# Optimization experiments

Measured on AMD Instinct MI355X. Metric: run time of the kernel, lower is better.

The kernel has to match this reference:

```python
import jax, jax.numpy as jnp
import numpy as np

B, T, C = 32, 128, 64
E, H = 8, 4            # feat_dim, num_heads
D = E // H             # head_dim = 2
HID = 32               # hidden_dim


def setup_inputs() -> dict:
    key = jax.random.key(0)
    ks = jax.random.split(key, 20)
    s = 0.1
    return {
        "x": jax.random.normal(ks[0], (B, T, C), jnp.float32),
        # input_proj: Linear(C, C)
        "W_in": jax.random.normal(ks[1], (C, C), jnp.float32) * s,
        "b_in": jax.random.normal(ks[2], (C,), jnp.float32) * s,
        # time_step_score: Linear(C, C//4) -> GELU -> Linear(C//4, 1) -> Sigmoid
        "W_ts1": jax.random.normal(ks[3], (C // 4, C), jnp.float32) * s,
        "b_ts1": jax.random.normal(ks[4], (C // 4,), jnp.float32) * s,
        "W_ts2": jax.random.normal(ks[5], (1, C // 4), jnp.float32) * s,
        "b_ts2": jax.random.normal(ks[6], (1,), jnp.float32) * s,
        # per-channel GRU(1 -> E): torch gate order (r, z, n)
        "W_ih": jax.random.normal(ks[7], (C, 3 * E), jnp.float32) * s,      # input size 1
        "W_hh": jax.random.normal(ks[8], (C, 3 * E, E), jnp.float32) * s,
        "b_ih": jax.random.normal(ks[9], (C, 3 * E), jnp.float32) * s,
        "b_hh": jax.random.normal(ks[10], (C, 3 * E), jnp.float32) * s,
        # shared MultiheadAttention(E, 4): packed in_proj + out_proj
        "W_qkv": jax.random.normal(ks[11], (3 * E, E), jnp.float32) * s,
        "b_qkv": jax.random.normal(ks[12], (3 * E,), jnp.float32) * s,
        "W_o": jax.random.normal(ks[13], (E, E), jnp.float32) * s,
        "b_o": jax.random.normal(ks[14], (E,), jnp.float32) * s,
        # out_proj: Linear(C*E, HID)
        "W_out": jax.random.normal(ks[15], (HID, C * E), jnp.float32) * s,
        "b_out": jax.random.normal(ks[16], (HID,), jnp.float32) * s,
    }


def _forward(x, W_in, b_in, W_ts1, b_ts1, W_ts2, b_ts2,
             W_ih, W_hh, b_ih, b_hh, W_qkv, b_qkv, W_o, b_o, W_out, b_out):
    bs, ts, c = x.shape
    # time step importance: per-timestep MLP over the raw features
    h1 = jax.nn.gelu(jnp.einsum('btc,fc->btf', x, W_ts1) + b_ts1, approximate=False)
    ts_imp = jax.nn.sigmoid(jnp.einsum('btf,of->bto', h1, W_ts2) + b_ts2)[..., 0]  # [B,T]

    xp = jnp.einsum('btc,dc->btd', x, W_in) + b_in  # [B,T,C]

    # Batched per-channel GRU scan over time. state h: [B,C,E]
    def step(h, x_t):
        gi = x_t[:, :, None] * W_ih[None] + b_ih          # [B,C,3E]
        gh = jnp.einsum('bce,cge->bcg', h, W_hh) + b_hh   # [B,C,3E]
        ir, iz, inn = gi[..., :E], gi[..., E:2 * E], gi[..., 2 * E:]
        hr, hz, hn = gh[..., :E], gh[..., E:2 * E], gh[..., 2 * E:]
        r = jax.nn.sigmoid(ir + hr)
        z = jax.nn.sigmoid(iz + hz)
        n = jnp.tanh(inn + r * hn)
        h_new = (1.0 - z) * n + z * h
        return h_new, h_new

    h0 = jnp.zeros((bs, c, E), xp.dtype)
    _, hs = jax.lax.scan(step, h0, jnp.transpose(xp, (1, 0, 2)))  # [T,B,C,E]
    hs_bcte = jnp.transpose(hs, (1, 2, 0, 3))                     # [B,C,T,E]

    # Shared MHA applied independently per channel (batched over B*C)
    qkv = jnp.einsum('bcte,fe->bctf', hs_bcte, W_qkv) + b_qkv     # [B,C,T,3E]
    q, k, v = qkv[..., :E], qkv[..., E:2 * E], qkv[..., 2 * E:]
    def heads(t):
        return t.reshape(bs, c, ts, H, D)
    q, k, v = heads(q), heads(k), heads(v)
    scores = jnp.einsum('bcthd,bcshd->bchts', q, k) / np.sqrt(D)
    attn = jax.nn.softmax(scores, axis=-1)
    o = jnp.einsum('bchts,bcshd->bcthd', attn, v).reshape(bs, c, ts, E)
    attn_out = jnp.einsum('bcte,fe->bctf', o, W_o) + b_o          # [B,C,T,E]
    attention = jnp.transpose(attn_out, (0, 2, 1, 3))             # [B,T,C,E]

    out_flat = jnp.transpose(hs, (1, 0, 2, 3)).reshape(bs, ts, c * E)  # [B,T,C*E]
    out = jnp.einsum('btf,hf->bth', out_flat, W_out) + b_out           # [B,T,HID]

    feat_imp = jax.nn.sigmoid(attention.sum(axis=(1, 3)))   # [B,C]
    tsf_imp = jax.nn.sigmoid(attention.sum(axis=-1))        # [B,T,C]
    return out[:, -1, :], feat_imp, ts_imp, tsf_imp


def reference(x, W_in, b_in, W_ts1, b_ts1, W_ts2, b_ts2,
              W_ih, W_hh, b_ih, b_hh, W_qkv, b_qkv, W_o, b_o, W_out, b_out):
    return _forward(x, W_in, b_in, W_ts1, b_ts1, W_ts2, b_ts2,
                    W_ih, W_hh, b_ih, b_hh, W_qkv, b_qkv, W_o, b_o, W_out, b_out)
```

## Files before the change

### kernel.cpp

```cpp
#include <hip/hip_runtime.h>
#include <hip/hip_bf16.h>
#include <math.h>

#define B_ 32
#define T_ 128
#define C_ 64
#define E_ 8
#define HID_ 32

#define LOG2E 1.44269504088896341f

__device__ __forceinline__ float fast_rcp(float x) { return __builtin_amdgcn_rcpf(x); }
__device__ __forceinline__ float fast_exp2(float x) { return exp2f(x); }
__device__ __forceinline__ float fast_sigmoid(float x) {
    return fast_rcp(1.0f + fast_exp2(-LOG2E * x));
}
__device__ __forceinline__ float fast_tanh(float x) {
    float xc = __builtin_amdgcn_fmed3f(x, -15.0f, 15.0f);
    float t = fast_exp2(2.0f * LOG2E * xc);
    return (t - 1.0f) * fast_rcp(t + 1.0f);
}

template <int CTRL>
__device__ __forceinline__ float dppf(float v) {
    return __int_as_float(__builtin_amdgcn_update_dpp(
        __float_as_int(v), __float_as_int(v), CTRL, 0xF, 0xF, false));
}
#define QP_XOR1 0xB1
#define QP_XOR2 0x4E
#define QP_XOR3 0x1B
#define HALF_MIRROR 0x141

__global__ __launch_bounds__(64) void k_pre_ts(
    const float* __restrict__ x, const float* __restrict__ W_in, const float* __restrict__ b_in,
    const float* __restrict__ W_ts1, const float* __restrict__ b_ts1,
    const float* __restrict__ W_ts2, const float* __restrict__ b_ts2,
    float* __restrict__ xp, float* __restrict__ ts_imp)
{
    const int bt = blockIdx.x;
    const int tid = threadIdx.x;
    __shared__ __align__(16) float xs[C_];
    __shared__ float h1[16];
    if (tid < 16) ((float4*)xs)[tid] = ((const float4*)(x + bt * C_))[tid];
    __syncthreads();

    float a = b_in[tid];
    const float4* w4 = (const float4*)(W_in + tid * C_);
#pragma unroll
    for (int k4 = 0; k4 < 16; ++k4) {
        float4 xv = ((const float4*)xs)[k4];
        float4 wv = w4[k4];
        a = fmaf(xv.x, wv.x, a); a = fmaf(xv.y, wv.y, a);
        a = fmaf(xv.z, wv.z, a); a = fmaf(xv.w, wv.w, a);
    }
    xp[bt * C_ + tid] = a;

    if (tid < 16) {
        float s = b_ts1[tid];
#pragma unroll
        for (int k = 0; k < C_; ++k) s = fmaf(xs[k], W_ts1[tid * C_ + k], s);
        h1[tid] = 0.5f * s * (1.0f + erff(s * 0.70710678118654752f));
    }
    __syncthreads();
    if (tid == 0) {
        float s = b_ts2[0];
#pragma unroll
        for (int k = 0; k < 16; ++k) s = fmaf(h1[k], W_ts2[k], s);
        ts_imp[bt] = fast_sigmoid(s);
    }
}

__global__ __launch_bounds__(64) void k_gru(
    const float* __restrict__ xp, const float* __restrict__ W_ih, const float* __restrict__ W_hh,
    const float* __restrict__ b_ih, const float* __restrict__ b_hh,
    float* __restrict__ hs, float* __restrict__ fh)
{
    const int tid = threadIdx.x;
    const int ci = tid >> 3;
    const int e = tid & 7;
    const int chain = blockIdx.x * 8 + ci;
    const int c = chain & 63;

    __shared__ float xc[8][T_ + 1];

    const int c_base = (blockIdx.x & 7) * 8;
    const int bb = blockIdx.x >> 3;
    for (int idx = tid; idx < 8 * T_; idx += 64) {
        int cci = idx & 7, t = idx >> 3;
        xc[cci][t] = xp[(bb * T_ + t) * C_ + c_base + cci];
    }
    __syncthreads();

    float wr[8], wz[8], wn[8];
#pragma unroll
    for (int m = 0; m < 8; ++m) {
        const int j = e ^ m;
        wr[m] = W_hh[(c * 24 + 0  + e) * 8 + j];
        wz[m] = W_hh[(c * 24 + 8  + e) * 8 + j];
        wn[m] = W_hh[(c * 24 + 16 + e) * 8 + j];
    }
    const float wir = W_ih[c * 24 + e], wiz = W_ih[c * 24 + 8 + e], win = W_ih[c * 24 + 16 + e];
    const float cr = b_ih[c * 24 + e] + b_hh[c * 24 + e];
    const float cz = b_ih[c * 24 + 8 + e] + b_hh[c * 24 + 8 + e];
    const float bin_ = b_ih[c * 24 + 16 + e];
    const float bhn  = b_hh[c * 24 + 16 + e];

    float h = 0.0f;
    float* ho = hs + (size_t)chain * T_ * E_ + e;
    float xv = xc[ci][0];
    for (int t = 0; t < T_; ++t) {
        float xvn = xc[ci][t + 1];
        float p1 = dppf<QP_XOR1>(h);
        float p2 = dppf<QP_XOR2>(h);
        float p3 = dppf<QP_XOR3>(h);
        float p7 = dppf<HALF_MIRROR>(h);
        float p6 = dppf<HALF_MIRROR>(p1);
        float p5 = dppf<HALF_MIRROR>(p2);
        float p4 = dppf<HALF_MIRROR>(p3);
        const float pa[8] = {h, p1, p2, p3, p4, p5, p6, p7};

        float g0 = fmaf(pa[1], wr[1], pa[0] * wr[0]);
        float g1 = fmaf(pa[3], wr[3], pa[2] * wr[2]);
        float g2 = fmaf(pa[5], wr[5], pa[4] * wr[4]);
        float g3 = fmaf(pa[7], wr[7], pa[6] * wr[6]);
        float gr = fmaf(xv, wir, cr) + ((g0 + g1) + (g2 + g3));
        float z0 = fmaf(pa[1], wz[1], pa[0] * wz[0]);
        float z1 = fmaf(pa[3], wz[3], pa[2] * wz[2]);
        float z2 = fmaf(pa[5], wz[5], pa[4] * wz[4]);
        float z3 = fmaf(pa[7], wz[7], pa[6] * wz[6]);
        float gz = fmaf(xv, wiz, cz) + ((z0 + z1) + (z2 + z3));
        float n0 = fmaf(pa[1], wn[1], pa[0] * wn[0]);
        float n1 = fmaf(pa[3], wn[3], pa[2] * wn[2]);
        float n2 = fmaf(pa[5], wn[5], pa[4] * wn[4]);
        float n3 = fmaf(pa[7], wn[7], pa[6] * wn[6]);
        float hn = bhn + ((n0 + n1) + (n2 + n3));
        float gn = fmaf(xv, win, bin_);
        float r = fast_sigmoid(gr);
        float z = fast_sigmoid(gz);
        float nn = fast_tanh(fmaf(r, hn, gn));
        h = fmaf(z, h - nn, nn);
        ho[t * E_] = h;
        xv = xvn;
    }
    fh[chain * E_ + e] = h;
}

__global__ __launch_bounds__(256) void k_attn(
    const float* __restrict__ hs, const float* __restrict__ W_qkv, const float* __restrict__ b_qkv,
    const float* __restrict__ W_o, const float* __restrict__ b_o,
    float* __restrict__ feat_imp, float* __restrict__ tsf_imp)
{
    const int bc = blockIdx.x;
    const int b = bc >> 6, c = bc & 63;
    const int tid = threadIdx.x;
    const int t2 = tid & 63;
    const int sq = tid >> 6;

    __shared__ __align__(16) float ks[T_][E_];
    __shared__ __align__(16) float us[T_][4];
    __shared__ float qsT[E_][T_];
    __shared__ float pacc[3][T_][8];
    __shared__ float red[T_];

    const float qscale = 0.70710678118654752f * LOG2E;

    {
        const int row = (tid < 128) ? tid : (tid - 128);
        const float4* hp = (const float4*)(hs + (size_t)bc * T_ * E_ + row * E_);
        float4 h0 = hp[0], h1 = hp[1];
        float hr[E_] = {h0.x, h0.y, h0.z, h0.w, h1.x, h1.y, h1.z, h1.w};
        if (tid < 128) {
            float kv[E_];
#pragma unroll
            for (int f = 0; f < E_; ++f) {
                float a = b_qkv[E_ + f];
#pragma unroll
                for (int j = 0; j < E_; ++j) a = fmaf(hr[j], W_qkv[(E_ + f) * E_ + j], a);
                kv[f] = a;
            }
            ((float4*)&ks[row][0])[0] = make_float4(kv[0], kv[1], kv[2], kv[3]);
            ((float4*)&ks[row][0])[1] = make_float4(kv[4], kv[5], kv[6], kv[7]);
#pragma unroll
            for (int f = 0; f < E_; ++f) {
                float a = b_qkv[f];
#pragma unroll
                for (int j = 0; j < E_; ++j) a = fmaf(hr[j], W_qkv[f * E_ + j], a);
                qsT[f][row] = a * qscale;
            }
        } else {
            float ws[E_];
#pragma unroll
            for (int d = 0; d < E_; ++d) {
                float wv = 0.0f;
#pragma unroll
                for (int fp = 0; fp < E_; ++fp) wv += W_o[fp * E_ + d];
                ws[d] = wv;
            }
            float vv[E_];
#pragma unroll
            for (int f = 0; f < E_; ++f) {
                float a = b_qkv[2 * E_ + f];
#pragma unroll
                for (int j = 0; j < E_; ++j) a = fmaf(hr[j], W_qkv[(2 * E_ + f) * E_ + j], a);
                vv[f] = a;
            }
            float4 uu;
            uu.x = fmaf(vv[1], ws[1], vv[0] * ws[0]);
            uu.y = fmaf(vv[3], ws[3], vv[2] * ws[2]);
            uu.z = fmaf(vv[5], ws[5], vv[4] * ws[4]);
            uu.w = fmaf(vv[7], ws[7], vv[6] * ws[6]);
            *((float4*)&us[row][0]) = uu;
        }
    }
    __syncthreads();

    float q0[E_], q1[E_];
#pragma unroll
    for (int f = 0; f < E_; ++f) { q0[f] = qsT[f][t2]; q1[f] = qsT[f][t2 + 64]; }

    float l0[4] = {0.f,0.f,0.f,0.f}, S0[4] = {0.f,0.f,0.f,0.f};
    float l1[4] = {0.f,0.f,0.f,0.f}, S1[4] = {0.f,0.f,0.f,0.f};
    const float* kb = &ks[sq * 32][0];
    const float* ub = &us[sq * 32][0];
#pragma unroll 8
    for (int i = 0; i < 32; ++i) {
        float4 k0 = *(const float4*)(kb + i * 8);
        float4 k1 = *(const float4*)(kb + i * 8 + 4);
        float4 uu = *(const float4*)(ub + i * 4);
        float p00 = fast_exp2(fmaf(q0[1], k0.y, q0[0] * k0.x));
        float p01 = fast_exp2(fmaf(q0[3], k0.w, q0[2] * k0.z));
        float p02 = fast_exp2(fmaf(q0[5], k1.y, q0[4] * k1.x));
        float p03 = fast_exp2(fmaf(q0[7], k1.w, q0[6] * k1.z));
        float p10 = fast_exp2(fmaf(q1[1], k0.y, q1[0] * k0.x));
        float p11 = fast_exp2(fmaf(q1[3], k0.w, q1[2] * k0.z));
        float p12 = fast_exp2(fmaf(q1[5], k1.y, q1[4] * k1.x));
        float p13 = fast_exp2(fmaf(q1[7], k1.w, q1[6] * k1.z));
        l0[0] += p00; l0[1] += p01; l0[2] += p02; l0[3] += p03;
        l1[0] += p10; l1[1] += p11; l1[2] += p12; l1[3] += p13;
        S0[0] = fmaf(p00, uu.x, S0[0]); S0[1] = fmaf(p01, uu.y, S0[1]);
        S0[2] = fmaf(p02, uu.z, S0[2]); S0[3] = fmaf(p03, uu.w, S0[3]);
        S1[0] = fmaf(p10, uu.x, S1[0]); S1[1] = fmaf(p11, uu.y, S1[1]);
        S1[2] = fmaf(p12, uu.z, S1[2]); S1[3] = fmaf(p13, uu.w, S1[3]);
    }

    if (sq > 0) {
        float* pr = &pacc[sq - 1][t2][0];
#pragma unroll
        for (int i = 0; i < 4; ++i) { pr[i] = l0[i]; pr[4 + i] = S0[i]; }
        pr = &pacc[sq - 1][t2 + 64][0];
#pragma unroll
        for (int i = 0; i < 4; ++i) { pr[i] = l1[i]; pr[4 + i] = S1[i]; }
    }
    __syncthreads();

    if (sq == 0) {
        float bsum = 0.0f;
#pragma unroll
        for (int fp = 0; fp < E_; ++fp) bsum += b_o[fp];
#pragma unroll
        for (int qq = 0; qq < 3; ++qq) {
#pragma unroll
            for (int i = 0; i < 4; ++i) {
                l0[i] += pacc[qq][t2][i];       S0[i] += pacc[qq][t2][4 + i];
                l1[i] += pacc[qq][t2 + 64][i];  S1[i] += pacc[qq][t2 + 64][4 + i];
            }
        }
        float Sa = bsum, Sb = bsum;
#pragma unroll
        for (int hh = 0; hh < 4; ++hh) {
            Sa = fmaf(S0[hh], fast_rcp(l0[hh]), Sa);
            Sb = fmaf(S1[hh], fast_rcp(l1[hh]), Sb);
        }
        tsf_imp[(size_t)b * T_ * C_ + (size_t)t2 * C_ + c] = fast_sigmoid(Sa);
        tsf_imp[(size_t)b * T_ * C_ + (size_t)(t2 + 64) * C_ + c] = fast_sigmoid(Sb);
        red[t2] = Sa;
        red[t2 + 64] = Sb;
    }
    __syncthreads();
    for (int off = 64; off > 0; off >>= 1) {
        if (tid < off) red[tid] += red[tid + off];
        __syncthreads();
    }
    if (tid == 0) feat_imp[bc] = fast_sigmoid(red[0]);
}

__global__ __launch_bounds__(64) void k_out(
    const float* __restrict__ fh, const float* __restrict__ W_out, const float* __restrict__ b_out,
    float* __restrict__ out0)
{
    const int b = blockIdx.x;
    const int tid = threadIdx.x;
    __shared__ float hf[C_ * E_];
    const float4* src = (const float4*)(fh + (b * C_ + tid) * E_);
    float4* dst = (float4*)(hf + tid * E_);
    dst[0] = src[0];
    dst[1] = src[1];
    __syncthreads();
    if (tid < HID_) {
        float a = b_out[tid];
        const float* wo = W_out + tid * (C_ * E_);
        for (int k = 0; k < C_ * E_; ++k) a = fmaf(hf[k], wo[k], a);
        out0[b * HID_ + tid] = a;
    }
}

extern "C" void kernel_launch(void* const* d_in, const int* in_sizes, int n_in,
                              void* d_out, int out_size, void* d_ws, size_t ws_size,
                              hipStream_t stream) {
    (void)in_sizes; (void)n_in; (void)out_size; (void)ws_size;

    float* out0 = (float*)d_out;
    float* feat = out0 + B_ * HID_;
    float* tsim = feat + B_ * C_;
    float* tsf  = tsim + B_ * T_;

    const float* x     = (const float*)d_in[0];
    const float* W_in  = (const float*)d_in[1];
    const float* b_in  = (const float*)d_in[2];
    const float* W_ts1 = (const float*)d_in[3];
    const float* b_ts1 = (const float*)d_in[4];
    const float* W_ts2 = (const float*)d_in[5];
    const float* b_ts2 = (const float*)d_in[6];
    const float* W_ih  = (const float*)d_in[7];
    const float* W_hh  = (const float*)d_in[8];
    const float* b_ih  = (const float*)d_in[9];
    const float* b_hh  = (const float*)d_in[10];
    const float* W_qkv = (const float*)d_in[11];
    const float* b_qkv = (const float*)d_in[12];
    const float* W_o   = (const float*)d_in[13];
    const float* b_o   = (const float*)d_in[14];
    const float* W_out = (const float*)d_in[15];
    const float* b_out = (const float*)d_in[16];

    float* fhb = (float*)d_ws;
    float* xpb = fhb + B_ * C_ * E_;
    float* hsb = xpb + (size_t)B_ * T_ * C_;

    hipLaunchKernelGGL(k_pre_ts, dim3(B_ * T_), dim3(64), 0, stream,
                       x, W_in, b_in, W_ts1, b_ts1, W_ts2, b_ts2, xpb, tsim);
    hipLaunchKernelGGL(k_gru, dim3(B_ * C_ / 8), dim3(64), 0, stream,
                       xpb, W_ih, W_hh, b_ih, b_hh, hsb, fhb);
    hipLaunchKernelGGL(k_out, dim3(B_), dim3(64), 0, stream,
                       fhb, W_out, b_out, out0);
    hipLaunchKernelGGL(k_attn, dim3(B_ * C_), dim3(256), 0, stream,
                       hsb, W_qkv, b_qkv, W_o, b_o, feat, tsf);
}
```

Measured before the change: 93.24 us.

## Split attention key range across lane pairs and reduce with shuffles

Each thread in the attention kernel now handles one query row and half of the keys (64), where before it handled two query rows over a quarter of the keys. Partial softmax sums are combined with a single xor-shuffle between paired lanes instead of a shared-memory partial buffer and an extra barrier. The feature-importance sum now uses wave shuffles plus a 4-entry shared array, replacing a 7-step shared-memory tree reduction with a barrier per step. This cuts LDS traffic and barriers, but each thread reuses a loaded K/V row for only one query, so LDS reads per exp go up.

```diff
diff --git a/kernel.cpp b/kernel.cpp
--- a/kernel.cpp
+++ b/kernel.cpp
@@ -153,20 +153,22 @@
     const int bc = blockIdx.x;
     const int b = bc >> 6, c = bc & 63;
     const int tid = threadIdx.x;
-    const int t2 = tid & 63;
-    const int sq = tid >> 6;
+    const int w = tid >> 6;
+    const int lane = tid & 63;
+    const int ri = lane >> 1;
+    const int sh = lane & 1;
+    const int row = w * 32 + ri;
 
     __shared__ __align__(16) float ks[T_][E_];
     __shared__ __align__(16) float us[T_][4];
     __shared__ float qsT[E_][T_];
-    __shared__ float pacc[3][T_][8];
-    __shared__ float red[T_];
+    __shared__ float red4[4];
 
     const float qscale = 0.70710678118654752f * LOG2E;
 
     {
-        const int row = (tid < 128) ? tid : (tid - 128);
-        const float4* hp = (const float4*)(hs + (size_t)bc * T_ * E_ + row * E_);
+        const int srow = (tid < 128) ? tid : (tid - 128);
+        const float4* hp = (const float4*)(hs + (size_t)bc * T_ * E_ + srow * E_);
         float4 h0 = hp[0], h1 = hp[1];
         float hr[E_] = {h0.x, h0.y, h0.z, h0.w, h1.x, h1.y, h1.z, h1.w};
         if (tid < 128) {
@@ -178,14 +180,14 @@
                 for (int j = 0; j < E_; ++j) a = fmaf(hr[j], W_qkv[(E_ + f) * E_ + j], a);
                 kv[f] = a;
             }
-            ((float4*)&ks[row][0])[0] = make_float4(kv[0], kv[1], kv[2], kv[3]);
-            ((float4*)&ks[row][0])[1] = make_float4(kv[4], kv[5], kv[6], kv[7]);
+            ((float4*)&ks[srow][0])[0] = make_float4(kv[0], kv[1], kv[2], kv[3]);
+            ((float4*)&ks[srow][0])[1] = make_float4(kv[4], kv[5], kv[6], kv[7]);
 #pragma unroll
             for (int f = 0; f < E_; ++f) {
                 float a = b_qkv[f];
 #pragma unroll
                 for (int j = 0; j < E_; ++j) a = fmaf(hr[j], W_qkv[f * E_ + j], a);
-                qsT[f][row] = a * qscale;
+                qsT[f][srow] = a * qscale;
             }
         } else {
             float ws[E_];
@@ -209,79 +211,58 @@
             uu.y = fmaf(vv[3], ws[3], vv[2] * ws[2]);
             uu.z = fmaf(vv[5], ws[5], vv[4] * ws[4]);
             uu.w = fmaf(vv[7], ws[7], vv[6] * ws[6]);
-            *((float4*)&us[row][0]) = uu;
+            *((float4*)&us[srow][0]) = uu;
         }
     }
     __syncthreads();
 
-    float q0[E_], q1[E_];
-#pragma unroll
-    for (int f = 0; f < E_; ++f) { q0[f] = qsT[f][t2]; q1[f] = qsT[f][t2 + 64]; }
-
-    float l0[4] = {0.f,0.f,0.f,0.f}, S0[4] = {0.f,0.f,0.f,0.f};
-    float l1[4] = {0.f,0.f,0.f,0.f}, S1[4] = {0.f,0.f,0.f,0.f};
-    const float* kb = &ks[sq * 32][0];
-    const float* ub = &us[sq * 32][0];
+    float q[E_];
+#pragma unroll
+    for (int f = 0; f < E_; ++f) q[f] = qsT[f][row];
+
+    float l[4] = {0.f, 0.f, 0.f, 0.f};
+    float S[4] = {0.f, 0.f, 0.f, 0.f};
+    const float* kb = &ks[sh * 64][0];
+    const float* ub = &us[sh * 64][0];
 #pragma unroll 8
-    for (int i = 0; i < 32; ++i) {
+    for (int i = 0; i < 64; ++i) {
         float4 k0 = *(const float4*)(kb + i * 8);
         float4 k1 = *(const float4*)(kb + i * 8 + 4);
         float4 uu = *(const float4*)(ub + i * 4);
-        float p00 = fast_exp2(fmaf(q0[1], k0.y, q0[0] * k0.x));
-        float p01 = fast_exp2(fmaf(q0[3], k0.w, q0[2] * k0.z));
-        float p02 = fast_exp2(fmaf(q0[5], k1.y, q0[4] * k1.x));
-        float p03 = fast_exp2(fmaf(q0[7], k1.w, q0[6] * k1.z));
-        float p10 = fast_exp2(fmaf(q1[1], k0.y, q1[0] * k0.x));
-        float p11 = fast_exp2(fmaf(q1[3], k0.w, q1[2] * k0.z));
-        float p12 = fast_exp2(fmaf(q1[5], k1.y, q1[4] * k1.x));
-        float p13 = fast_exp2(fmaf(q1[7], k1.w, q1[6] * k1.z));
-        l0[0] += p00; l0[1] += p01; l0[2] += p02; l0[3] += p03;
-        l1[0] += p10; l1[1] += p11; l1[2] += p12; l1[3] += p13;
-        S0[0] = fmaf(p00, uu.x, S0[0]); S0[1] = fmaf(p01, uu.y, S0[1]);
-        S0[2] = fmaf(p02, uu.z, S0[2]); S0[3] = fmaf(p03, uu.w, S0[3]);
-        S1[0] = fmaf(p10, uu.x, S1[0]); S1[1] = fmaf(p11, uu.y, S1[1]);
-        S1[2] = fmaf(p12, uu.z, S1[2]); S1[3] = fmaf(p13, uu.w, S1[3]);
-    }
-
-    if (sq > 0) {
-        float* pr = &pacc[sq - 1][t2][0];
-#pragma unroll
-        for (int i = 0; i < 4; ++i) { pr[i] = l0[i]; pr[4 + i] = S0[i]; }
-        pr = &pacc[sq - 1][t2 + 64][0];
-#pragma unroll
-        for (int i = 0; i < 4; ++i) { pr[i] = l1[i]; pr[4 + i] = S1[i]; }
-    }
-    __syncthreads();
-
-    if (sq == 0) {
-        float bsum = 0.0f;
-#pragma unroll
-        for (int fp = 0; fp < E_; ++fp) bsum += b_o[fp];
-#pragma unroll
-        for (int qq = 0; qq < 3; ++qq) {
-#pragma unroll
-            for (int i = 0; i < 4; ++i) {
-                l0[i] += pacc[qq][t2][i];       S0[i] += pacc[qq][t2][4 + i];
-                l1[i] += pacc[qq][t2 + 64][i];  S1[i] += pacc[qq][t2 + 64][4 + i];
-            }
-        }
-        float Sa = bsum, Sb = bsum;
-#pragma unroll
-        for (int hh = 0; hh < 4; ++hh) {
-            Sa = fmaf(S0[hh], fast_rcp(l0[hh]), Sa);
-            Sb = fmaf(S1[hh], fast_rcp(l1[hh]), Sb);
-        }
-        tsf_imp[(size_t)b * T_ * C_ + (size_t)t2 * C_ + c] = fast_sigmoid(Sa);
-        tsf_imp[(size_t)b * T_ * C_ + (size_t)(t2 + 64) * C_ + c] = fast_sigmoid(Sb);
-        red[t2] = Sa;
-        red[t2 + 64] = Sb;
-    }
-    __syncthreads();
-    for (int off = 64; off > 0; off >>= 1) {
-        if (tid < off) red[tid] += red[tid + off];
-        __syncthreads();
-    }
-    if (tid == 0) feat_imp[bc] = fast_sigmoid(red[0]);
+        float p0 = fast_exp2(fmaf(q[1], k0.y, q[0] * k0.x));
+        float p1 = fast_exp2(fmaf(q[3], k0.w, q[2] * k0.z));
+        float p2 = fast_exp2(fmaf(q[5], k1.y, q[4] * k1.x));
+        float p3 = fast_exp2(fmaf(q[7], k1.w, q[6] * k1.z));
+        l[0] += p0; l[1] += p1; l[2] += p2; l[3] += p3;
+        S[0] = fmaf(p0, uu.x, S[0]);
+        S[1] = fmaf(p1, uu.y, S[1]);
+        S[2] = fmaf(p2, uu.z, S[2]);
+        S[3] = fmaf(p3, uu.w, S[3]);
+    }
+
+#pragma unroll
+    for (int i = 0; i < 4; ++i) {
+        l[i] += __shfl_xor(l[i], 1);
+        S[i] += __shfl_xor(S[i], 1);
+    }
+
+    float bsum = 0.0f;
+#pragma unroll
+    for (int fp = 0; fp < E_; ++fp) bsum += b_o[fp];
+    float Sv = bsum;
+#pragma unroll
+    for (int hh = 0; hh < 4; ++hh) Sv = fmaf(S[hh], fast_rcp(l[hh]), Sv);
+
+    if (sh == 0)
+        tsf_imp[(size_t)b * T_ * C_ + (size_t)row * C_ + c] = fast_sigmoid(Sv);
+
+    float fsum = Sv;
+#pragma unroll
+    for (int off = 2; off <= 32; off <<= 1) fsum += __shfl_xor(fsum, off);
+    if (lane == 0) red4[w] = fsum;
+    __syncthreads();
+    if (tid == 0)
+        feat_imp[bc] = fast_sigmoid(red4[0] + red4[1] + red4[2] + red4[3]);
 }
 
 __global__ __launch_bounds__(64) void k_out(
```

Result: no change. 92.91 us (-0.4%).

## Restructure attention kernel to 128 threads with lane-pair key split and shuffle reductions

Applied to the files above, without the earlier changes.

Shrinks the attention block from 256 to 128 threads. Each thread now computes all of Q, K and the V-derived projection for one row. The key range is split across adjacent lane pairs, using two interleaved padded LDS buffers, and each thread processes two query rows over 64 keys. The cross-quarter shared-memory partial-sum exchange and the tree reduction are replaced by wavefront shuffles plus a single barrier. This removes several barriers and LDS traffic, but doubles per-thread loop length and the per-thread projection work, and reduces threads per block.

```diff
diff --git a/kernel.cpp b/kernel.cpp
--- a/kernel.cpp
+++ b/kernel.cpp
@@ -145,7 +145,7 @@
     fh[chain * E_ + e] = h;
 }
 
-__global__ __launch_bounds__(256) void k_attn(
+__global__ __launch_bounds__(128) void k_attn(
     const float* __restrict__ hs, const float* __restrict__ W_qkv, const float* __restrict__ b_qkv,
     const float* __restrict__ W_o, const float* __restrict__ b_o,
     float* __restrict__ feat_imp, float* __restrict__ tsf_imp)
@@ -153,77 +153,78 @@
     const int bc = blockIdx.x;
     const int b = bc >> 6, c = bc & 63;
     const int tid = threadIdx.x;
-    const int t2 = tid & 63;
-    const int sq = tid >> 6;
-
-    __shared__ __align__(16) float ks[T_][E_];
-    __shared__ __align__(16) float us[T_][4];
+    const int w = tid >> 6;
+    const int lane = tid & 63;
+    const int ri = lane >> 1;
+    const int sh = lane & 1;
+    const int row0 = w * 64 + ri;
+    const int row1 = w * 64 + 32 + ri;
+
+    __shared__ __align__(16) float ks[2][516];
+    __shared__ __align__(16) float us[2][260];
     __shared__ float qsT[E_][T_];
-    __shared__ float pacc[3][T_][8];
-    __shared__ float red[T_];
+    __shared__ float red2[2];
 
     const float qscale = 0.70710678118654752f * LOG2E;
 
     {
-        const int row = (tid < 128) ? tid : (tid - 128);
-        const float4* hp = (const float4*)(hs + (size_t)bc * T_ * E_ + row * E_);
+        const int srow = tid;
+        const float4* hp = (const float4*)(hs + (size_t)bc * T_ * E_ + srow * E_);
         float4 h0 = hp[0], h1 = hp[1];
         float hr[E_] = {h0.x, h0.y, h0.z, h0.w, h1.x, h1.y, h1.z, h1.w};
-        if (tid < 128) {
-            float kv[E_];
-#pragma unroll
-            for (int f = 0; f < E_; ++f) {
-                float a = b_qkv[E_ + f];
-#pragma unroll
-                for (int j = 0; j < E_; ++j) a = fmaf(hr[j], W_qkv[(E_ + f) * E_ + j], a);
-                kv[f] = a;
-            }
-            ((float4*)&ks[row][0])[0] = make_float4(kv[0], kv[1], kv[2], kv[3]);
-            ((float4*)&ks[row][0])[1] = make_float4(kv[4], kv[5], kv[6], kv[7]);
-#pragma unroll
-            for (int f = 0; f < E_; ++f) {
-                float a = b_qkv[f];
-#pragma unroll
-                for (int j = 0; j < E_; ++j) a = fmaf(hr[j], W_qkv[f * E_ + j], a);
-                qsT[f][row] = a * qscale;
-            }
-        } else {
-            float ws[E_];
-#pragma unroll
-            for (int d = 0; d < E_; ++d) {
-                float wv = 0.0f;
-#pragma unroll
-                for (int fp = 0; fp < E_; ++fp) wv += W_o[fp * E_ + d];
-                ws[d] = wv;
-            }
-            float vv[E_];
-#pragma unroll
-            for (int f = 0; f < E_; ++f) {
-                float a = b_qkv[2 * E_ + f];
-#pragma unroll
-                for (int j = 0; j < E_; ++j) a = fmaf(hr[j], W_qkv[(2 * E_ + f) * E_ + j], a);
-                vv[f] = a;
-            }
-            float4 uu;
-            uu.x = fmaf(vv[1], ws[1], vv[0] * ws[0]);
-            uu.y = fmaf(vv[3], ws[3], vv[2] * ws[2]);
-            uu.z = fmaf(vv[5], ws[5], vv[4] * ws[4]);
-            uu.w = fmaf(vv[7], ws[7], vv[6] * ws[6]);
-            *((float4*)&us[row][0]) = uu;
+        float* kdst = &ks[srow >> 6][(srow & 63) * 8];
+        float kv[E_];
+#pragma unroll
+        for (int f = 0; f < E_; ++f) {
+            float a = b_qkv[E_ + f];
+#pragma unroll
+            for (int j = 0; j < E_; ++j) a = fmaf(hr[j], W_qkv[(E_ + f) * E_ + j], a);
+            kv[f] = a;
         }
+        ((float4*)kdst)[0] = make_float4(kv[0], kv[1], kv[2], kv[3]);
+        ((float4*)kdst)[1] = make_float4(kv[4], kv[5], kv[6], kv[7]);
+#pragma unroll
+        for (int f = 0; f < E_; ++f) {
+            float a = b_qkv[f];
+#pragma unroll
+            for (int j = 0; j < E_; ++j) a = fmaf(hr[j], W_qkv[f * E_ + j], a);
+            qsT[f][srow] = a * qscale;
+        }
+        float ws[E_];
+#pragma unroll
+        for (int d = 0; d < E_; ++d) {
+            float wv = 0.0f;
+#pragma unroll
+            for (int fp = 0; fp < E_; ++fp) wv += W_o[fp * E_ + d];
+            ws[d] = wv;
+        }
+        float vv[E_];
+#pragma unroll
+        for (int f = 0; f < E_; ++f) {
+            float a = b_qkv[2 * E_ + f];
+#pragma unroll
+            for (int j = 0; j < E_; ++j) a = fmaf(hr[j], W_qkv[(2 * E_ + f) * E_ + j], a);
+            vv[f] = a;
+        }
+        float4 uu;
+        uu.x = fmaf(vv[1], ws[1], vv[0] * ws[0]);
+        uu.y = fmaf(vv[3], ws[3], vv[2] * ws[2]);
+        uu.z = fmaf(vv[5], ws[5], vv[4] * ws[4]);
+        uu.w = fmaf(vv[7], ws[7], vv[6] * ws[6]);
+        *((float4*)&us[srow >> 6][(srow & 63) * 4]) = uu;
     }
     __syncthreads();
 
     float q0[E_], q1[E_];
 #pragma unroll
-    for (int f = 0; f < E_; ++f) { q0[f] = qsT[f][t2]; q1[f] = qsT[f][t2 + 64]; }
+    for (int f = 0; f < E_; ++f) { q0[f] = qsT[f][row0]; q1[f] = qsT[f][row1]; }
 
     float l0[4] = {0.f,0.f,0.f,0.f}, S0[4] = {0.f,0.f,0.f,0.f};
     float l1[4] = {0.f,0.f,0.f,0.f}, S1[4] = {0.f,0.f,0.f,0.f};
-    const float* kb = &ks[sq * 32][0];
-    const float* ub = &us[sq * 32][0];
+    const float* kb = &ks[sh][0];
+    const float* ub = &us[sh][0];
 #pragma unroll 8
-    for (int i = 0; i < 32; ++i) {
+    for (int i = 0; i < 64; ++i) {
         float4 k0 = *(const float4*)(kb + i * 8);
         float4 k1 = *(const float4*)(kb + i * 8 + 4);
         float4 uu = *(const float4*)(ub + i * 4);
@@ -243,45 +244,33 @@
         S1[2] = fmaf(p12, uu.z, S1[2]); S1[3] = fmaf(p13, uu.w, S1[3]);
     }
 
-    if (sq > 0) {
-        float* pr = &pacc[sq - 1][t2][0];
-#pragma unroll
-        for (int i = 0; i < 4; ++i) { pr[i] = l0[i]; pr[4 + i] = S0[i]; }
-        pr = &pacc[sq - 1][t2 + 64][0];
-#pragma unroll
-        for (int i = 0; i < 4; ++i) { pr[i] = l1[i]; pr[4 + i] = S1[i]; }
-    }
-    __syncthreads();
-
-    if (sq == 0) {
-        float bsum = 0.0f;
-#pragma unroll
-        for (int fp = 0; fp < E_; ++fp) bsum += b_o[fp];
-#pragma unroll
-        for (int qq = 0; qq < 3; ++qq) {
-#pragma unroll
-            for (int i = 0; i < 4; ++i) {
-                l0[i] += pacc[qq][t2][i];       S0[i] += pacc[qq][t2][4 + i];
-                l1[i] += pacc[qq][t2 + 64][i];  S1[i] += pacc[qq][t2 + 64][4 + i];
-            }
-        }
-        float Sa = bsum, Sb = bsum;
-#pragma unroll
-        for (int hh = 0; hh < 4; ++hh) {
-            Sa = fmaf(S0[hh], fast_rcp(l0[hh]), Sa);
-            Sb = fmaf(S1[hh], fast_rcp(l1[hh]), Sb);
-        }
-        tsf_imp[(size_t)b * T_ * C_ + (size_t)t2 * C_ + c] = fast_sigmoid(Sa);
-        tsf_imp[(size_t)b * T_ * C_ + (size_t)(t2 + 64) * C_ + c] = fast_sigmoid(Sb);
-        red[t2] = Sa;
-        red[t2 + 64] = Sb;
-    }
-    __syncthreads();
-    for (int off = 64; off > 0; off >>= 1) {
-        if (tid < off) red[tid] += red[tid + off];
-        __syncthreads();
-    }
-    if (tid == 0) feat_imp[bc] = fast_sigmoid(red[0]);
+#pragma unroll
+    for (int i = 0; i < 4; ++i) {
+        l0[i] += __shfl_xor(l0[i], 1);  S0[i] += __shfl_xor(S0[i], 1);
+        l1[i] += __shfl_xor(l1[i], 1);  S1[i] += __shfl_xor(S1[i], 1);
+    }
+
+    float bsum = 0.0f;
+#pragma unroll
+    for (int fp = 0; fp < E_; ++fp) bsum += b_o[fp];
+    float Sa = bsum, Sb = bsum;
+#pragma unroll
+    for (int hh = 0; hh < 4; ++hh) {
+        Sa = fmaf(S0[hh], fast_rcp(l0[hh]), Sa);
+        Sb = fmaf(S1[hh], fast_rcp(l1[hh]), Sb);
+    }
+
+    if (sh == 0) {
+        tsf_imp[(size_t)b * T_ * C_ + (size_t)row0 * C_ + c] = fast_sigmoid(Sa);
+        tsf_imp[(size_t)b * T_ * C_ + (size_t)row1 * C_ + c] = fast_sigmoid(Sb);
+    }
+
+    float fsum = Sa + Sb;
+#pragma unroll
+    for (int off = 2; off <= 32; off <<= 1) fsum += __shfl_xor(fsum, off);
+    if (lane == 0) red2[w] = fsum;
+    __syncthreads();
+    if (tid == 0) feat_imp[bc] = fast_sigmoid(red2[0] + red2[1]);
 }
 
 __global__ __launch_bounds__(64) void k_out(
@@ -342,6 +331,6 @@
                        xpb, W_ih, W_hh, b_ih, b_hh, hsb, fhb);
     hipLaunchKernelGGL(k_out, dim3(B_), dim3(64), 0, stream,
                        fhb, W_out, b_out, out0);
-    hipLaunchKernelGGL(k_attn, dim3(B_ * C_), dim3(256), 0, stream,
+    hipLaunchKernelGGL(k_attn, dim3(B_ * C_), dim3(128), 0, stream,
                        hsb, W_qkv, b_qkv, W_o, b_o, feat, tsf);
 }
```

Result: no change. 94.26 us (+1.1%).
